# Kernel tuning notes

Hardware: AMD Instinct MI355X
Metric: run time of the kernel (lower is better)

Reference implementation:

```python
import jax, jax.numpy as jnp
import numpy as np

N = 50000      # nodes
E = 800000     # edges (before self loops)
DIN = 128      # input_dim
H = 128        # hidden_dim
DOUT = 64      # output_dim
G = 64         # graphs in batch
EATTR = 16     # edge_attr dim (unused by math, kept for signature fidelity)


def _conv_params(key, din, h, scale=0.05):
    ks = jax.random.split(key, 6)
    return dict(
        lin_w=jax.random.normal(ks[0], (din, h), dtype=jnp.float32) * scale,
        lin_b=jnp.zeros((h,), jnp.float32),
        w1=jax.random.normal(ks[1], (2 * h, h), dtype=jnp.float32) * scale,
        b1=jnp.zeros((h,), jnp.float32),
        w2=jax.random.normal(ks[2], (h, h), dtype=jnp.float32) * scale,
        b2=jnp.zeros((h,), jnp.float32),
    )


def setup_inputs() -> dict:
    key = jax.random.key(0)
    ks = jax.random.split(key, 10)
    inp = {
        'x': jax.random.normal(ks[0], (N, DIN), dtype=jnp.float32),
        'edge_index': jax.random.randint(ks[1], (2, E), 0, N),
        'edge_attr': jax.random.normal(ks[2], (E, EATTR), dtype=jnp.float32),
        'batch': jnp.sort(jax.random.randint(ks[3], (N,), 0, G)),
    }
    p1 = _conv_params(ks[4], DIN, H)
    p2 = _conv_params(ks[5], H, H)
    p3 = _conv_params(ks[6], H, H)
    for i, p in enumerate((p1, p2, p3), start=1):
        for k, v in p.items():
            inp[f'c{i}_{k}'] = v
    inp['out_w'] = jax.random.normal(ks[7], (H, DOUT), dtype=jnp.float32) * 0.05
    inp['out_b'] = jnp.zeros((DOUT,), jnp.float32)
    return inp


def mpnn_conv(x, src, dst, lin_w, lin_b, w1, b1, w2, b2):
    # x: [N, din] -> h: [N, H]
    n = x.shape[0]
    h = x @ lin_w + lin_b
    loop = jnp.arange(n)
    s = jnp.concatenate([src, loop])   # x_j (source) indices, self loops appended
    d = jnp.concatenate([dst, loop])   # x_i (target) indices
    z = jnp.concatenate([h[d], h[s]], axis=-1)          # [E+N, 2H]  (cat[x_i, x_j])
    m = jax.nn.relu(z @ w1 + b1) @ w2 + b2              # [E+N, H]
    return jax.ops.segment_sum(m, d, num_segments=n)    # aggr='add' at targets


def reference(x, edge_index, edge_attr, batch,
              c1_lin_w, c1_lin_b, c1_w1, c1_b1, c1_w2, c1_b2,
              c2_lin_w, c2_lin_b, c2_w1, c2_b1, c2_w2, c2_b2,
              c3_lin_w, c3_lin_b, c3_w1, c3_b1, c3_w2, c3_b2,
              out_w, out_b):
    src, dst = edge_index[0], edge_index[1]
    h = jax.nn.relu(mpnn_conv(x, src, dst, c1_lin_w, c1_lin_b, c1_w1, c1_b1, c1_w2, c1_b2))
    h = jax.nn.relu(mpnn_conv(h, src, dst, c2_lin_w, c2_lin_b, c2_w1, c2_b1, c2_w2, c2_b2))
    h = jax.nn.relu(mpnn_conv(h, src, dst, c3_lin_w, c3_lin_b, c3_w1, c3_b1, c3_w2, c3_b2))
    # global_mean_pool over graphs
    sums = jax.ops.segment_sum(h, batch, num_segments=G)                       # [G, H]
    cnts = jax.ops.segment_sum(jnp.ones((h.shape[0],), h.dtype), batch, num_segments=G)
    pooled = sums / jnp.maximum(cnts, 1.0)[:, None]
    return pooled @ out_w + out_b
```

## Files before the change

### kernel.cpp

```cpp
#include <hip/hip_runtime.h>
#include <hip/hip_bf16.h>


typedef _Float16 f16_t;
typedef f16_t f16x2 __attribute__((ext_vector_type(2)));
typedef f16_t f16x8 __attribute__((ext_vector_type(8)));
typedef float f32x4 __attribute__((ext_vector_type(4)));
typedef float f32x2v __attribute__((ext_vector_type(2)));
typedef unsigned int u32;
typedef unsigned short u16;
typedef unsigned char u8;

__device__ __forceinline__ float f16lo(u32 v) {
    return (float)__builtin_bit_cast(f16_t, (u16)(v & 0xffff));
}
__device__ __forceinline__ float f16hi(u32 v) {
    return (float)__builtin_bit_cast(f16_t, (u16)(v >> 16));
}
__device__ __forceinline__ u16 f16b(float x) { return __builtin_bit_cast(u16, (f16_t)x); }
__device__ __forceinline__ u32 f16pack(float x, float y) {
    return (u32)f16b(x) | ((u32)f16b(y) << 16);
}

typedef __attribute__((address_space(1))) void gvoid_t;
typedef __attribute__((address_space(3))) void lvoid_t;
__device__ __forceinline__ void glds16(const void* g, void* l) {
    __builtin_amdgcn_global_load_lds((gvoid_t*)g, (lvoid_t*)l, 16, 0, 0);
}

struct PrepArgs {
    const float* x; f16_t* xb; int totalx;
    const int* ei; int E;
    int* hist; int nbk; int NB;
    const float* lin_w[3]; const float* lin_b[3];
    const float* w1[3]; const float* b1[3]; const float* w2[3];
    f16_t* linw16;
    f16_t* w1T;
    f16_t* W2t;
    float* bias256c;
};

__global__ __launch_bounds__(256) void prep_kernel(PrepArgs A, int nConvB) {
    __shared__ union { int hist[512]; u16 T16[128 * 130]; } shm;
    const int b = blockIdx.x, tid = threadIdx.x;
    const int nTr = 9, nLw = 48, nBias = 3;
    if (b < nTr) {
        int layer = b / 3, which = b % 3;
        const float* src; f16_t* dst;
        if (which == 0)      { src = A.w1[layer];          dst = A.w1T + layer * 32768; }
        else if (which == 1) { src = A.w1[layer] + 16384;  dst = A.w1T + layer * 32768 + 16384; }
        else                 { src = A.w2[layer];          dst = A.W2t + layer * 16384; }
#pragma unroll
        for (int it = 0; it < 16; ++it) {
            int idx = it * 1024 + tid * 4;
            int r = idx >> 7, c = idx & 127;
            float4 v = *(const float4*)(src + idx);
            *(u32*)&shm.T16[r * 130 + c] = f16pack(v.x, v.y);
            *(u32*)&shm.T16[r * 130 + c + 2] = f16pack(v.z, v.w);
        }
        __syncthreads();
#pragma unroll
        for (int it = 0; it < 32; ++it) {
            int o = it * 256 + tid;
            int j = o >> 6, c = (o & 63) * 2;
            u32 w = (u32)shm.T16[c * 130 + j] | ((u32)shm.T16[(c + 1) * 130 + j] << 16);
            ((u32*)dst)[o] = w;
        }
        return;
    }
    if (b < nTr + nLw) {
        int i = (b - nTr) * 1024 + tid * 4;
        int layer = i >> 14, off = i & 16383;
        float4 v = *(const float4*)(A.lin_w[layer] + off);
        *(uint2*)(A.linw16 + i) = make_uint2(f16pack(v.x, v.y), f16pack(v.z, v.w));
        return;
    }
    if (b < nTr + nLw + nBias) {
        int layer = b - nTr - nLw;
        int j = tid;
        const float* w1p = A.w1[layer];
        const float* wcol = (j < 128) ? (w1p + j) : (w1p + 16384 + (j - 128));
        const float* lbp = A.lin_b[layer];
        float s = (j < 128) ? A.b1[layer][j] : 0.f;
        for (int c = 0; c < 128; ++c) s += lbp[c] * wcol[c * 128];
        A.bias256c[layer * 256 + j] = s;
        return;
    }
    if (b < nTr + nLw + nBias + A.NB) {
        const int bb = b - nTr - nLw - nBias;
        const int nbk = A.nbk, E = A.E;
        for (int i = tid; i < nbk; i += 256) shm.hist[i] = 0;
        __syncthreads();
        const int chunk = (E + A.NB - 1) / A.NB;
        const int e0 = bb * chunk, e1 = min(E, e0 + chunk);
        for (int e = e0 + tid; e < e1; e += 256) atomicAdd(&shm.hist[A.ei[E + e] >> 7], 1);
        __syncthreads();
        for (int i = tid; i < nbk; i += 256) A.hist[(size_t)bb * nbk + i] = shm.hist[i];
        return;
    }
    int i = ((b - nTr - nLw - nBias - A.NB) * 256 + tid) * 4;
    if (i >= A.totalx) return;
    float4 v = *(const float4*)(A.x + i);
    *(uint2*)(A.xb + i) = make_uint2(f16pack(v.x, v.y), f16pack(v.z, v.w));
}

__global__ __launch_bounds__(256) void hscan_kernel(int* __restrict__ hist,
                                                    int* __restrict__ bcnt, int nbk, int NB) {
    __shared__ int sh[256];
    const int b = blockIdx.x, t = threadIdx.x;
    int run = 0;
    for (int c0 = 0; c0 < NB; c0 += 256) {
        int idx = c0 + t;
        int v = (idx < NB) ? hist[(size_t)idx * nbk + b] : 0;
        sh[t] = v;
        __syncthreads();
#pragma unroll
        for (int o = 1; o < 256; o <<= 1) {
            int u = (t >= o) ? sh[t - o] : 0;
            __syncthreads();
            sh[t] += u;
            __syncthreads();
        }
        if (idx < NB) hist[(size_t)idx * nbk + b] = run + sh[t] - v;
        int tot = sh[255];
        __syncthreads();
        run += tot;
    }
    if (t == 0) bcnt[b] = run;
}

__global__ __launch_bounds__(256) void scat_kernel(const int* __restrict__ ei,
                                                   const int* __restrict__ hist,
                                                   u32* __restrict__ bbuf, int E, int NB,
                                                   int nbk, int cap) {
    __shared__ int basep[512];
    __shared__ int cnt2[512];
    const int bb = blockIdx.x, t = threadIdx.x;
    for (int i = t; i < nbk; i += 256) {
        basep[i] = hist[(size_t)bb * nbk + i];
        cnt2[i] = 0;
    }
    __syncthreads();
    const int chunk = (E + NB - 1) / NB;
    const int e0 = bb * chunk, e1 = min(E, e0 + chunk);
    for (int e = e0 + t; e < e1; e += 256) {
        int dst = ei[E + e], src = ei[e];
        int bkt = dst >> 7;
        int r = atomicAdd(&cnt2[bkt], 1);
        int pp = basep[bkt] + r;
        if (pp < cap) bbuf[(size_t)bkt * cap + pp] = ((u32)(dst & 127) << 16) | (u32)src;
    }
}

__global__ __launch_bounds__(128) void part2_kernel(const u32* __restrict__ bbuf,
                                                    const int* __restrict__ bcnt,
                                                    int* __restrict__ row_ptr,
                                                    float* __restrict__ cntp1f,
                                                    int* __restrict__ bsumB, int cap, int N) {
    __shared__ int ldeg[128];
    __shared__ int sh[128];
    const int b = blockIdx.x, t = threadIdx.x;
    ldeg[t] = 0;
    __syncthreads();
    const int cnt = min(bcnt[b], cap);
    const u32* p = bbuf + (size_t)b * cap;
    for (int i = t; i < cnt; i += 128) atomicAdd(&ldeg[p[i] >> 16], 1);
    __syncthreads();
    int d = ldeg[t];
    sh[t] = d;
    __syncthreads();
#pragma unroll
    for (int o = 1; o < 128; o <<= 1) {
        int u = (t >= o) ? sh[t - o] : 0;
        __syncthreads();
        sh[t] += u;
        __syncthreads();
    }
    int node = (b << 7) + t;
    if (node < N) {
        row_ptr[node] = sh[t] - d;
        cntp1f[node] = (float)(d + 1);
    }
    if (t == 127) bsumB[b] = sh[127];
}

__global__ __launch_bounds__(512) void scanb_kernel(const int* __restrict__ bsumB,
                                                    int* __restrict__ bbase,
                                                    int* __restrict__ row_ptr, int nbk, int N) {
    __shared__ int sh[512];
    const int t = threadIdx.x;
    int v = (t < nbk) ? bsumB[t] : 0;
    sh[t] = v;
    __syncthreads();
#pragma unroll
    for (int o = 1; o < 512; o <<= 1) {
        int u = (t >= o) ? sh[t - o] : 0;
        __syncthreads();
        sh[t] += u;
        __syncthreads();
    }
    if (t < nbk) bbase[t] = sh[t] - v;
    if (t == 511) row_ptr[N] = sh[511];
}

__global__ __launch_bounds__(128) void part3_kernel(const u32* __restrict__ bbuf,
                                                    const int* __restrict__ bcnt,
                                                    const int* __restrict__ bbase,
                                                    int* __restrict__ row_ptr,
                                                    u16* __restrict__ colarr, int cap, int N) {
    __shared__ int lcur[128];
    const int b = blockIdx.x, t = threadIdx.x;
    const int node = (b << 7) + t;
    const int bb = bbase[b];
    int rp = 0;
    if (node < N) {
        rp = row_ptr[node] + bb;
        row_ptr[node] = rp;
    }
    lcur[t] = rp;
    __syncthreads();
    const int cnt = min(bcnt[b], cap);
    const u32* p = bbuf + (size_t)b * cap;
    for (int i = t; i < cnt; i += 128) {
        u32 en = p[i];
        int addr = atomicAdd(&lcur[en >> 16], 1);
        colarr[addr] = (u16)(en & 0xffffu);
    }
}

__device__ __forceinline__ void gemm_tile(const f16_t* __restrict__ X,
                                          const f16_t* __restrict__ Wt,
                                          f16_t* __restrict__ Y, int N,
                                          int ldc, int row0) {
    __shared__ f16_t sX[128 * 128];
    __shared__ f16_t sW[128 * 128];
    const int tid = threadIdx.x;
    const int wave = tid >> 6, lane = tid & 63;
#pragma unroll
    for (int it = 0; it < 8; ++it) {
        int idx = it * 256 + tid;
        int r = idx >> 4, c8 = idx & 15;
        int gr = row0 + r;
        if (gr >= N) gr = 0;
        glds16(X + (size_t)gr * 128 + ((c8 ^ (r & 7)) * 8),
               sX + (size_t)(it * 256 + (wave << 6)) * 8);
    }
#pragma unroll
    for (int it = 0; it < 8; ++it) {
        int idx = it * 256 + tid;
        int r = idx >> 4, c8 = idx & 15;
        glds16(Wt + (size_t)r * 128 + ((c8 ^ (r & 7)) * 8),
               sW + (size_t)(it * 256 + (wave << 6)) * 8);
    }
    __syncthreads();
    const int m = lane & 15, q = lane >> 4;
    const int sw = m & 7;
    f32x4 acc[2][8];
#pragma unroll
    for (int rt = 0; rt < 2; ++rt)
#pragma unroll
        for (int t = 0; t < 8; ++t) acc[rt][t] = (f32x4){0.f, 0.f, 0.f, 0.f};
#pragma unroll
    for (int kk = 0; kk < 4; ++kk) {
        const int g = (kk * 4 + q) ^ sw;
        f16x8 a0 = *(const f16x8*)(&sX[(wave * 32 + m) * 128 + g * 8]);
        f16x8 a1 = *(const f16x8*)(&sX[(wave * 32 + 16 + m) * 128 + g * 8]);
#pragma unroll
        for (int t = 0; t < 8; ++t) {
            f16x8 bfr = *(const f16x8*)(&sW[(t * 16 + m) * 128 + g * 8]);
            acc[0][t] = __builtin_amdgcn_mfma_f32_16x16x32_f16(a0, bfr, acc[0][t], 0, 0, 0);
            acc[1][t] = __builtin_amdgcn_mfma_f32_16x16x32_f16(a1, bfr, acc[1][t], 0, 0, 0);
        }
    }
#pragma unroll
    for (int t = 0; t < 8; ++t) {
        int col = t * 16 + m;
#pragma unroll
        for (int rt = 0; rt < 2; ++rt) {
#pragma unroll
            for (int j = 0; j < 4; ++j) {
                int r = row0 + wave * 32 + rt * 16 + q * 4 + j;
                if (r < N) Y[(size_t)r * ldc + col] = (f16_t)acc[rt][t][j];
            }
        }
    }
}

__global__ __launch_bounds__(256) void compose_kernel(const f16_t* __restrict__ w1T,
                                                      const f16_t* __restrict__ linw16,
                                                      f16_t* __restrict__ W12ct) {
    int layer = blockIdx.x >> 1, rb = blockIdx.x & 1;
    gemm_tile(w1T + layer * 32768, linw16 + layer * 16384, W12ct + layer * 32768, 256, 128,
              rb * 128);
}

template <int NT>
__global__ __launch_bounds__(512, 1) void gemm_persist(
    const f16_t* __restrict__ X, const f16_t* __restrict__ Wt,
    const float* __restrict__ bias, const float* __restrict__ bias2,
    const float* __restrict__ rowscale, f16_t* __restrict__ Y, u8* __restrict__ Y8,
    int N, int relu_flag, int ntiles) {
    __shared__ f16_t sW[NT * 16 * 128];
    __shared__ f16_t sX[2][128 * 128];
    const int tid = threadIdx.x;
    const int wave = tid >> 6, lane = tid & 63;
    const int m = lane & 15, q = lane >> 4, sw = m & 7;
    constexpr int NR = (NT == 16) ? 2 : 1;
    const int rb0 = (NT == 16) ? ((wave & 3) * 32) : (wave * 16);
    const int chalf = (NT == 16) ? (wave >> 2) : 0;

#pragma unroll
    for (int it = 0; it < NT / 2; ++it) {
        int idx = it * 512 + tid;
        int r = idx >> 4, c8 = idx & 15;
        glds16(Wt + (size_t)r * 128 + ((c8 ^ (r & 7)) * 8),
               sW + (size_t)(it * 512 + (wave << 6)) * 8);
    }
    float bvv[8], b2vv[8];
#pragma unroll
    for (int t2 = 0; t2 < 8; ++t2) {
        int colb = chalf * 128 + t2 * 16 + m;
        bvv[t2] = bias ? bias[colb] : 0.f;
        b2vv[t2] = bias2 ? bias2[colb] : 0.f;
    }
    int t = blockIdx.x;
    {
        int row0 = t * 128;
#pragma unroll
        for (int it = 0; it < 4; ++it) {
            int idx = it * 512 + tid;
            int r = idx >> 4, c8 = idx & 15;
            int gr = row0 + r;
            if (gr >= N) gr = 0;
            glds16(X + (size_t)gr * 128 + ((c8 ^ (r & 7)) * 8),
                   sX[0] + (size_t)(it * 512 + (wave << 6)) * 8);
        }
    }
    __syncthreads();
    int cur = 0;
    for (; t < ntiles; t += gridDim.x) {
        const int row0 = t * 128;
        const int tn = t + gridDim.x;
        f16_t* sXc = sX[cur];
        if (tn < ntiles) {
            const int r0n = tn * 128;
            f16_t* sXn = sX[cur ^ 1];
#pragma unroll
            for (int it = 0; it < 4; ++it) {
                int idx = it * 512 + tid;
                int r = idx >> 4, c8 = idx & 15;
                int gr = r0n + r;
                if (gr >= N) gr = 0;
                glds16(X + (size_t)gr * 128 + ((c8 ^ (r & 7)) * 8),
                       sXn + (size_t)(it * 512 + (wave << 6)) * 8);
            }
        }
        f32x4 acc[NR][8];
#pragma unroll
        for (int rt = 0; rt < NR; ++rt)
#pragma unroll
            for (int t2 = 0; t2 < 8; ++t2) acc[rt][t2] = (f32x4){0.f, 0.f, 0.f, 0.f};
#pragma unroll
        for (int kk = 0; kk < 4; ++kk) {
            const int g = (kk * 4 + q) ^ sw;
            f16x8 a0 = *(const f16x8*)(&sXc[(rb0 + m) * 128 + g * 8]);
            f16x8 a1{};
            if constexpr (NR == 2) a1 = *(const f16x8*)(&sXc[(rb0 + 16 + m) * 128 + g * 8]);
#pragma unroll
            for (int t2 = 0; t2 < 8; ++t2) {
                f16x8 bfr =
                    *(const f16x8*)(&sW[(size_t)(chalf * 128 + t2 * 16 + m) * 128 + g * 8]);
                acc[0][t2] = __builtin_amdgcn_mfma_f32_16x16x32_f16(a0, bfr, acc[0][t2], 0, 0, 0);
                if constexpr (NR == 2)
                    acc[1][t2] =
                        __builtin_amdgcn_mfma_f32_16x16x32_f16(a1, bfr, acc[1][t2], 0, 0, 0);
            }
        }
        if (NT == 16) __syncthreads();
        f16_t* region = sXc + wave * 16 * 128;
#pragma unroll
        for (int rt = 0; rt < NR; ++rt) {
            float rs[4];
#pragma unroll
            for (int j = 0; j < 4; ++j) {
                int gr = row0 + rb0 + rt * 16 + q * 4 + j;
                rs[j] = (bias2 && gr < N) ? rowscale[gr] : 0.f;
            }
#pragma unroll
            for (int t2 = 0; t2 < 8; ++t2) {
#pragma unroll
                for (int j = 0; j < 4; ++j) {
                    int rl2 = q * 4 + j;
                    float v = acc[rt][t2][j] + bvv[t2];
                    if (bias2) v += rs[j] * b2vv[t2];
                    if (relu_flag) v = fmaxf(v, 0.f);
                    region[rl2 * 128 + ((t2 * 16 + m) ^ ((rl2 & 4) << 3))] = (f16_t)v;
                }
            }
#pragma unroll
            for (int it2 = 0; it2 < 4; ++it2) {
                int i = it2 * 64 + lane;
                int rl = i >> 4, c8 = i & 15;
                int gr = row0 + rb0 + rt * 16 + rl;
                const f16_t* rp = &region[rl * 128 + ((c8 ^ (rl & 4)) * 8)];
                if (NT == 16 && chalf == 1) {
                    const u32* p = (const u32*)rp;
                    u32 lo = __builtin_amdgcn_cvt_pk_fp8_f32(f16lo(p[0]), f16hi(p[0]), 0u, false);
                    lo = __builtin_amdgcn_cvt_pk_fp8_f32(f16lo(p[1]), f16hi(p[1]), lo, true);
                    u32 hi = __builtin_amdgcn_cvt_pk_fp8_f32(f16lo(p[2]), f16hi(p[2]), 0u, false);
                    hi = __builtin_amdgcn_cvt_pk_fp8_f32(f16lo(p[3]), f16hi(p[3]), hi, true);
                    if (gr < N) *(uint2*)(Y8 + (size_t)gr * 128 + c8 * 8) = make_uint2(lo, hi);
                } else {
                    uint4 v4 = *(const uint4*)rp;
                    if (gr < N) *(uint4*)(Y + (size_t)gr * 128 + c8 * 8) = v4;
                }
            }
        }
        __syncthreads();
        cur ^= 1;
    }
}

__global__ __launch_bounds__(256) void gather_kernel(const f16_t* __restrict__ aArr,
                                                     const u8* __restrict__ b8,
                                                     const int* __restrict__ row_ptr,
                                                     const u16* __restrict__ colarr,
                                                     f16_t* __restrict__ q, int N) {
    int wid = (blockIdx.x * 256 + threadIdx.x) >> 6;
    int lane = threadIdx.x & 63;
    if (wid >= N) return;
    const int g = lane >> 4, l = lane & 15;
    uint4 A = ((const uint4*)aArr)[(size_t)wid * 16 + l];
    float a0 = f16lo(A.x), a1 = f16hi(A.x), a2 = f16lo(A.y), a3 = f16hi(A.y);
    float a4 = f16lo(A.z), a5 = f16hi(A.z), a6 = f16lo(A.w), a7 = f16hi(A.w);
    float c0 = 0.f, c1 = 0.f, c2 = 0.f, c3 = 0.f, c4 = 0.f, c5 = 0.f, c6 = 0.f, c7 = 0.f;
    const uint2* b8u = (const uint2*)b8;
    auto accum = [&](uint2 B) {
        f32x2v p0 = __builtin_amdgcn_cvt_pk_f32_fp8(B.x, false);
        f32x2v p1 = __builtin_amdgcn_cvt_pk_f32_fp8(B.x, true);
        f32x2v p2 = __builtin_amdgcn_cvt_pk_f32_fp8(B.y, false);
        f32x2v p3 = __builtin_amdgcn_cvt_pk_f32_fp8(B.y, true);
        c0 += fmaxf(a0 + p0.x, 0.f); c1 += fmaxf(a1 + p0.y, 0.f);
        c2 += fmaxf(a2 + p1.x, 0.f); c3 += fmaxf(a3 + p1.y, 0.f);
        c4 += fmaxf(a4 + p2.x, 0.f); c5 += fmaxf(a5 + p2.y, 0.f);
        c6 += fmaxf(a6 + p3.x, 0.f); c7 += fmaxf(a7 + p3.y, 0.f);
    };
    if (g == 0) accum(b8u[(size_t)wid * 16 + l]);
    int e0 = row_ptr[wid], e1 = row_ptr[wid + 1];
    int e = e0;
    for (; e + 16 <= e1; e += 16) {
        int s0 = colarr[e + g], s1 = colarr[e + 4 + g];
        int s2 = colarr[e + 8 + g], s3 = colarr[e + 12 + g];
        uint2 B0 = b8u[(size_t)s0 * 16 + l];
        uint2 B1 = b8u[(size_t)s1 * 16 + l];
        uint2 B2 = b8u[(size_t)s2 * 16 + l];
        uint2 B3 = b8u[(size_t)s3 * 16 + l];
        accum(B0); accum(B1); accum(B2); accum(B3);
    }
    for (; e < e1; e += 4) {
        int i0 = e + g;
        if (i0 < e1) accum(b8u[(size_t)colarr[i0] * 16 + l]);
    }
#pragma unroll
    for (int off = 16; off < 64; off <<= 1) {
        c0 += __shfl_xor(c0, off); c1 += __shfl_xor(c1, off);
        c2 += __shfl_xor(c2, off); c3 += __shfl_xor(c3, off);
        c4 += __shfl_xor(c4, off); c5 += __shfl_xor(c5, off);
        c6 += __shfl_xor(c6, off); c7 += __shfl_xor(c7, off);
    }
    if (g == 0) {
        uint4 o;
        o.x = f16pack(c0, c1); o.y = f16pack(c2, c3);
        o.z = f16pack(c4, c5); o.w = f16pack(c6, c7);
        ((uint4*)q)[(size_t)wid * 16 + l] = o;
    }
}

__global__ __launch_bounds__(256) void pool_kernel(const f16_t* __restrict__ agg,
                                                   const int* __restrict__ batch,
                                                   float* __restrict__ pooled,
                                                   int* __restrict__ cntg, int N) {
    int wid = (blockIdx.x * 256 + threadIdx.x) >> 6;
    int lane = threadIdx.x & 63;
    int n0 = wid * 32;
    if (n0 >= N) return;
    int n1 = min(n0 + 32, N);
    const u32* au = (const u32*)agg;
    int gcur = batch[n0];
    float sx = 0.f, sy = 0.f;
    int cnt = 0;
    for (int n = n0; n < n1; ++n) {
        int g = batch[n];
        if (g != gcur) {
            atomicAdd(&pooled[gcur * 128 + lane * 2], sx);
            atomicAdd(&pooled[gcur * 128 + lane * 2 + 1], sy);
            if (lane == 0) atomicAdd(&cntg[gcur], cnt);
            gcur = g; sx = 0.f; sy = 0.f; cnt = 0;
        }
        u32 v = au[(size_t)n * 64 + lane];
        sx += f16lo(v);
        sy += f16hi(v);
        ++cnt;
    }
    atomicAdd(&pooled[gcur * 128 + lane * 2], sx);
    atomicAdd(&pooled[gcur * 128 + lane * 2 + 1], sy);
    if (lane == 0) atomicAdd(&cntg[gcur], cnt);
}

__global__ __launch_bounds__(256) void final_kernel(const float* __restrict__ pooled,
                                                    const int* __restrict__ cntg,
                                                    const float* __restrict__ out_w,
                                                    const float* __restrict__ out_b,
                                                    float* __restrict__ out, int total) {
    int idx = blockIdx.x * 256 + threadIdx.x;
    if (idx >= total) return;
    int g = idx >> 6, o = idx & 63;
    float c = fmaxf((float)cntg[g], 1.0f);
    float s = 0.f;
#pragma unroll 4
    for (int k = 0; k < 128; ++k) s += pooled[g * 128 + k] * out_w[k * 64 + o];
    out[idx] = s / c + out_b[o];
}

extern "C" void kernel_launch(void* const* d_in, const int* in_sizes, int n_in, void* d_out,
                              int out_size, void* d_ws, size_t ws_size, hipStream_t stream) {
    const float* x = (const float*)d_in[0];
    const int* ei = (const int*)d_in[1];
    const int* batch = (const int*)d_in[3];
    const float* cw[3][6];
    for (int l = 0; l < 3; ++l)
        for (int j = 0; j < 6; ++j) cw[l][j] = (const float*)d_in[4 + l * 6 + j];
    const float* out_w = (const float*)d_in[22];
    const float* out_b = (const float*)d_in[23];
    float* out = (float*)d_out;

    const int N = in_sizes[0] / 128;
    const int E = in_sizes[1] / 2;
    const int G = out_size / 64;
    const int nbk = (N + 127) >> 7;
    const int NB = 416;
    const int cap = E / nbk + 512;

    char* base = (char*)d_ws;
    size_t off = 0;
    auto alloc = [&](size_t b) { size_t o = off; off += (b + 255) & ~(size_t)255; return o; };
    float* pooled = (float*)(base + alloc((size_t)G * 128 * 4));
    int* cntg = (int*)(base + alloc((size_t)G * 4));
    const size_t zero_bytes = off;
    int* hist = (int*)(base + alloc((size_t)NB * nbk * 4));
    int* bcnt = (int*)(base + alloc((size_t)nbk * 4));
    int* bsumB = (int*)(base + alloc((size_t)nbk * 4));
    int* bbase = (int*)(base + alloc((size_t)nbk * 4));
    int* row_ptr = (int*)(base + alloc((size_t)(N + 1) * 4));
    float* cntp1f = (float*)(base + alloc((size_t)N * 4));
    u16* colarr = (u16*)(base + alloc((size_t)E * 2));
    u32* bbuf = (u32*)(base + alloc((size_t)nbk * cap * 4));
    f16_t* xb = (f16_t*)(base + alloc((size_t)N * 128 * 2));
    f16_t* q = (f16_t*)(base + alloc((size_t)N * 128 * 2));
    f16_t* aArr = (f16_t*)(base + alloc((size_t)N * 128 * 2));
    u8* b8 = (u8*)(base + alloc((size_t)N * 128));
    f16_t* linw16 = (f16_t*)(base + alloc(3 * 16384 * 2));
    f16_t* w1T = (f16_t*)(base + alloc(3 * 32768 * 2));
    f16_t* W12ct = (f16_t*)(base + alloc(3 * 32768 * 2));
    f16_t* W2t = (f16_t*)(base + alloc(3 * 16384 * 2));
    float* bias256c = (float*)(base + alloc(3 * 256 * 4));
    (void)ws_size; (void)n_in;

    hipMemsetAsync(d_ws, 0, zero_bytes, stream);

    PrepArgs pa;
    pa.x = x; pa.xb = xb; pa.totalx = N * 128;
    pa.ei = ei; pa.E = E;
    pa.hist = hist; pa.nbk = nbk; pa.NB = NB;
    for (int l = 0; l < 3; ++l) {
        pa.lin_w[l] = cw[l][0]; pa.lin_b[l] = cw[l][1];
        pa.w1[l] = cw[l][2]; pa.b1[l] = cw[l][3]; pa.w2[l] = cw[l][4];
    }
    pa.linw16 = linw16; pa.w1T = w1T; pa.W2t = W2t; pa.bias256c = bias256c;
    const int nConvB = (N * 128 / 4 + 255) / 256;
    prep_kernel<<<9 + 48 + 3 + NB + nConvB, 256, 0, stream>>>(pa, nConvB);

    compose_kernel<<<6, 256, 0, stream>>>(w1T, linw16, W12ct);

    hscan_kernel<<<nbk, 256, 0, stream>>>(hist, bcnt, nbk, NB);
    scat_kernel<<<NB, 256, 0, stream>>>(ei, hist, bbuf, E, NB, nbk, cap);
    part2_kernel<<<nbk, 128, 0, stream>>>(bbuf, bcnt, row_ptr, cntp1f, bsumB, cap, N);
    scanb_kernel<<<1, 512, 0, stream>>>(bsumB, bbase, row_ptr, nbk, N);
    part3_kernel<<<nbk, 128, 0, stream>>>(bbuf, bcnt, bbase, row_ptr, colarr, cap, N);

    const int ntiles = (N + 127) >> 7;
    const int pgrid = (ntiles < 256) ? ntiles : 256;
    const f16_t* Xin = xb;
    for (int l = 0; l < 3; ++l) {
        gemm_persist<16><<<pgrid, 512, 0, stream>>>(Xin, W12ct + l * 32768,
                                                    bias256c + l * 256, nullptr, nullptr,
                                                    aArr, b8, N, 0, ntiles);
        gather_kernel<<<(N * 64 + 255) / 256, 256, 0, stream>>>(aArr, b8, row_ptr, colarr, q, N);
        gemm_persist<8><<<pgrid, 512, 0, stream>>>(q, W2t + l * 16384, nullptr, cw[l][5],
                                                   cntp1f, xb, nullptr, N, 1, ntiles);
        Xin = xb;
    }

    pool_kernel<<<((N + 31) / 32 * 64 + 255) / 256, 256, 0, stream>>>(Xin, batch, pooled, cntg, N);
    final_kernel<<<(G * 64 + 255) / 256, 256, 0, stream>>>(pooled, cntg, out_w, out_b, out,
                                                           G * 64);
}
```

Before: 387.8 us.

## Unify gather edge loop with clamped loads, shrink pool chunks, split final matvec

The gather loop now handles every edge in one unrolled 16-wide loop. Indices are clamped so all four loads are always issued, and the remainder case is predicated instead of running a separate serial tail. The pool kernel processes 8 nodes per wave instead of 32, giving more parallelism at the cost of more atomics. The final kernel uses one block per graph, splits the K=128 reduction over four wave partitions and combines them through shared memory. These target tail latency in the gather and underutilization in the small pooling and output stages.

```diff
diff --git a/kernel.cpp b/kernel.cpp
--- a/kernel.cpp
+++ b/kernel.cpp
@@ -446,20 +446,15 @@
         c6 += fmaxf(a6 + p3.x, 0.f); c7 += fmaxf(a7 + p3.y, 0.f);
     };
     if (g == 0) accum(b8u[(size_t)wid * 16 + l]);
-    int e0 = row_ptr[wid], e1 = row_ptr[wid + 1];
-    int e = e0;
-    for (; e + 16 <= e1; e += 16) {
-        int s0 = colarr[e + g], s1 = colarr[e + 4 + g];
-        int s2 = colarr[e + 8 + g], s3 = colarr[e + 12 + g];
-        uint2 B0 = b8u[(size_t)s0 * 16 + l];
-        uint2 B1 = b8u[(size_t)s1 * 16 + l];
-        uint2 B2 = b8u[(size_t)s2 * 16 + l];
-        uint2 B3 = b8u[(size_t)s3 * 16 + l];
-        accum(B0); accum(B1); accum(B2); accum(B3);
-    }
-    for (; e < e1; e += 4) {
-        int i0 = e + g;
-        if (i0 < e1) accum(b8u[(size_t)colarr[i0] * 16 + l]);
+    const int e0 = row_ptr[wid], e1 = row_ptr[wid + 1];
+    for (int e = e0; e < e1; e += 16) {
+#pragma unroll
+        for (int s = 0; s < 4; ++s) {
+            int idx = e + s * 4 + g;
+            int src = colarr[min(idx, e1 - 1)];
+            uint2 B = b8u[(size_t)src * 16 + l];
+            if (idx < e1) accum(B);
+        }
     }
 #pragma unroll
     for (int off = 16; off < 64; off <<= 1) {
@@ -482,9 +477,9 @@
                                                    int* __restrict__ cntg, int N) {
     int wid = (blockIdx.x * 256 + threadIdx.x) >> 6;
     int lane = threadIdx.x & 63;
-    int n0 = wid * 32;
+    int n0 = wid * 8;
     if (n0 >= N) return;
-    int n1 = min(n0 + 32, N);
+    int n1 = min(n0 + 8, N);
     const u32* au = (const u32*)agg;
     int gcur = batch[n0];
     float sx = 0.f, sy = 0.f;
@@ -511,15 +506,23 @@
                                                     const int* __restrict__ cntg,
                                                     const float* __restrict__ out_w,
                                                     const float* __restrict__ out_b,
-                                                    float* __restrict__ out, int total) {
-    int idx = blockIdx.x * 256 + threadIdx.x;
-    if (idx >= total) return;
-    int g = idx >> 6, o = idx & 63;
-    float c = fmaxf((float)cntg[g], 1.0f);
+                                                    float* __restrict__ out) {
+    __shared__ float red[256];
+    const int g = blockIdx.x, tid = threadIdx.x;
+    const int o = tid & 63, part = tid >> 6;
     float s = 0.f;
-#pragma unroll 4
-    for (int k = 0; k < 128; ++k) s += pooled[g * 128 + k] * out_w[k * 64 + o];
-    out[idx] = s / c + out_b[o];
+#pragma unroll
+    for (int kk = 0; kk < 32; ++kk) {
+        int k = part * 32 + kk;
+        s += pooled[g * 128 + k] * out_w[k * 64 + o];
+    }
+    red[tid] = s;
+    __syncthreads();
+    if (part == 0) {
+        float c = fmaxf((float)cntg[g], 1.0f);
+        float tot = red[o] + red[o + 64] + red[o + 128] + red[o + 192];
+        out[g * 64 + o] = tot / c + out_b[o];
+    }
 }
 
 extern "C" void kernel_launch(void* const* d_in, const int* in_sizes, int n_in, void* d_out,
@@ -601,7 +604,6 @@
         Xin = xb;
     }
 
-    pool_kernel<<<((N + 31) / 32 * 64 + 255) / 256, 256, 0, stream>>>(Xin, batch, pooled, cntg, N);
-    final_kernel<<<(G * 64 + 255) / 256, 256, 0, stream>>>(pooled, cntg, out_w, out_b, out,
-                                                           G * 64);
-}
+    pool_kernel<<<((N + 7) / 8 * 64 + 255) / 256, 256, 0, stream>>>(Xin, batch, pooled, cntg, N);
+    final_kernel<<<G, 256, 0, stream>>>(pooled, cntg, out_w, out_b, out);
+}
```

New measurement: 413.6 us. +6.6%, slower.
